# Kernel tuning notes

Hardware: AMD Instinct MI355X
Metric: run time of the kernel (lower is better)

## Reference

```python
import jax, jax.numpy as jnp
import numpy as np
from jax import lax

E = 4        # n_subnets
CAP = 48     # padded per-subnet batch (subnet_bs)
NB = 4       # subnet_num_block (ResBlocks per subnet)
F = 32       # num_feature
RES_SCALE = 0.1


def _conv(x, w, b):
    # x: [B,C,H,W], w: [O,I,3,3] -> SAME conv, NCHW
    y = lax.conv_general_dilated(x, w, (1, 1), 'SAME',
                                 dimension_numbers=('NCHW', 'OIHW', 'NCHW'))
    return y + b[None, :, None, None]


def _pixel_shuffle(x, r):
    B, C, H, W = x.shape
    c = C // (r * r)
    x = x.reshape(B, c, r, r, H, W)
    x = x.transpose(0, 1, 4, 2, 5, 3)          # [B,c,H,r,W,r]
    return x.reshape(B, c, H * r, W * r)


def _subnet(x, hw, hb, r1w, r1b, r2w, r2b, ew, eb, u1w, u1b, u2w, u2b, tw, tb):
    # x: [CAP,3,32,32] -> [CAP,3,128,128]
    h = _conv(x, hw, hb)                        # head
    res = h
    for i in range(NB):                         # ResBlocks: x + s*conv(relu(conv(x)))
        t = jax.nn.relu(_conv(res, r1w[i], r1b[i]))
        res = res + RES_SCALE * _conv(t, r2w[i], r2b[i])
    res = _conv(res, ew, eb) + h                # body_end + skip
    u = _pixel_shuffle(_conv(res, u1w, u1b), 2) # upscale x2
    u = _pixel_shuffle(_conv(u, u2w, u2b), 2)   # upscale x2
    return _conv(u, tw, tb)                     # tail


def setup_inputs() -> dict:
    key = jax.random.key(0)
    ks = jax.random.split(key, 24)

    def w(k, shape, fan_in):
        return jax.random.normal(k, shape, jnp.float32) * (1.0 / np.sqrt(fan_in))

    d = {}
    d['inputs'] = jax.random.normal(ks[0], (128, 3, 32, 32), jnp.float32)
    # classifier: conv3->32 + relu + GAP + linear 32->E
    d['cls_w'] = w(ks[1], (32, 3, 3, 3), 27)
    d['cls_b'] = jnp.zeros((32,), jnp.float32)
    d['cls_fw'] = w(ks[2], (E, 32), 32)
    d['cls_fb'] = jnp.zeros((E,), jnp.float32)
    # stacked per-expert subnet params (leading dim E)
    d['head_w'] = w(ks[3], (E, F, 3, 3, 3), 27)
    d['head_b'] = jnp.zeros((E, F), jnp.float32)
    d['rb_w1'] = w(ks[4], (E, NB, F, F, 3, 3), F * 9)
    d['rb_b1'] = jnp.zeros((E, NB, F), jnp.float32)
    d['rb_w2'] = w(ks[5], (E, NB, F, F, 3, 3), F * 9)
    d['rb_b2'] = jnp.zeros((E, NB, F), jnp.float32)
    d['end_w'] = w(ks[6], (E, F, F, 3, 3), F * 9)
    d['end_b'] = jnp.zeros((E, F), jnp.float32)
    d['up_w1'] = w(ks[7], (E, 4 * F, F, 3, 3), F * 9)
    d['up_b1'] = jnp.zeros((E, 4 * F), jnp.float32)
    d['up_w2'] = w(ks[8], (E, 4 * F, F, 3, 3), F * 9)
    d['up_b2'] = jnp.zeros((E, 4 * F), jnp.float32)
    d['tail_w'] = w(ks[9], (E, 3, F, 3, 3), F * 9)
    d['tail_b'] = jnp.zeros((E, 3), jnp.float32)
    return d


def reference(inputs, cls_w, cls_b, cls_fw, cls_fb, head_w, head_b,
              rb_w1, rb_b1, rb_w2, rb_b2, end_w, end_b,
              up_w1, up_b1, up_w2, up_b2, tail_w, tail_b):
    N = inputs.shape[0]
    # classifier scores -> hard routing (argmax)
    c = jax.nn.relu(_conv(inputs, cls_w, cls_b)).mean((2, 3))   # [N,32]
    scores = c @ cls_fw.T + cls_fb                              # [N,E]
    assign = jnp.argmax(scores, axis=-1)                        # [N]

    # scatter: per-expert sorted position lists, padded to CAP (sentinel N)
    pos = jnp.where(assign[None, :] == jnp.arange(E)[:, None],
                    jnp.arange(N)[None, :], N)                  # [E,N]
    pos = jnp.sort(pos, axis=1)[:, :CAP]                        # [E,CAP]
    valid = pos < N
    safe = jnp.minimum(pos, N - 1)
    x_all = inputs[safe] * valid[:, :, None, None, None]        # [E,CAP,3,32,32]

    # horizontally-fused experts via vmap over expert dim
    y_all = jax.vmap(_subnet)(x_all, head_w, head_b, rb_w1, rb_b1, rb_w2, rb_b2,
                              end_w, end_b, up_w1, up_b1, up_w2, up_b2,
                              tail_w, tail_b)                   # [E,CAP,3,128,128]

    # gather: place real rows back at their original batch positions
    y_all = y_all * valid[:, :, None, None, None]
    out = jnp.zeros((N, 3, 128, 128), y_all.dtype)
    out = out.at[safe.reshape(-1)].add(y_all.reshape(-1, 3, 128, 128))
    return out
```

## Files before the change

kernel.cpp:

```cpp
#include <hip/hip_runtime.h>

#define EXPN 4
#define CAP 48
#define NSLOT 192
#define NBLK 4

#define OFF_RB1 0
#define OFF_RB2 36864
#define OFF_END 73728
#define OFF_UP1 82944
#define OFF_UP2 119808
#define OFF_TAIL 156672
#define PER_E 157536

typedef __attribute__((ext_vector_type(8))) short bf16x8;
typedef __attribute__((ext_vector_type(4))) float f32x4;

static __device__ __forceinline__ float bf2f(unsigned short s) {
  union { unsigned u; float f; } c; c.u = ((unsigned)s) << 16; return c.f;
}
static __device__ __forceinline__ unsigned short f2bf(float f) {
  union { float f; unsigned u; } c; c.f = f;
  unsigned u = c.u;
  return (unsigned short)((u + 0x7fffu + ((u >> 16) & 1u)) >> 16);
}
static __device__ __forceinline__ f32x4 mfma16(bf16x8 a, bf16x8 b, f32x4 c) {
  return __builtin_amdgcn_mfma_f32_16x16x32_bf16(a, b, c, 0, 0, 0);
}
static __device__ __forceinline__ float relu_f(float x) { return fmaxf(x, 0.f); }

static __device__ __forceinline__ unsigned swz(unsigned p, unsigned s) {
  return p * 32 + ((s ^ ((p >> 1) & 3u)) * 8);
}

__global__ void k_zero(float4* __restrict__ p, int n4) {
  int i = blockIdx.x * blockDim.x + threadIdx.x;
  int stride = gridDim.x * blockDim.x;
  for (; i < n4; i += stride) p[i] = make_float4(0.f, 0.f, 0.f, 0.f);
}

__global__ __launch_bounds__(256) void k_wxform(
    const float* __restrict__ rb_w1, const float* __restrict__ rb_w2,
    const float* __restrict__ end_w, const float* __restrict__ up_w1,
    const float* __restrict__ up_w2, const float* __restrict__ tail_w,
    unsigned short* __restrict__ wt) {
  int idx = blockIdx.x * 256 + threadIdx.x;
  if (idx >= EXPN * PER_E) return;
  int e = idx / PER_E, r = idx % PER_E;
  const float* src;
  int c, OC;
  if (r < OFF_RB2) {
    int i = r / 9216; c = r % 9216; OC = 32;
    src = rb_w1 + ((size_t)e * NBLK + i) * 9216;
  } else if (r < OFF_END) {
    int i = (r - OFF_RB2) / 9216; c = (r - OFF_RB2) % 9216; OC = 32;
    src = rb_w2 + ((size_t)e * NBLK + i) * 9216;
  } else if (r < OFF_UP1) {
    c = r - OFF_END; OC = 32;
    src = end_w + (size_t)e * 9216;
  } else if (r < OFF_UP2) {
    c = r - OFF_UP1; OC = 128;
    src = up_w1 + (size_t)e * 36864;
  } else if (r < OFF_TAIL) {
    c = r - OFF_UP2; OC = 128;
    src = up_w2 + (size_t)e * 36864;
  } else {
    c = r - OFF_TAIL; OC = 3;
    src = tail_w + (size_t)e * 864;
  }
  int tap = c / (OC * 32);
  int rem = c % (OC * 32);
  int och = rem / 32, ich = rem % 32;
  wt[idx] = f2bf(src[(och * 32 + ich) * 9 + tap]);
}

__global__ __launch_bounds__(256) void k_cls_conv(
    const float* __restrict__ x, const float* __restrict__ cw,
    const float* __restrict__ cb, float* __restrict__ part) {
  int n = blockIdx.y, band = blockIdx.x, t = threadIdx.x;
  int og = t >> 6, r = (t >> 3) & 7, cg = t & 7;
  int c0 = cg * 4;
  __shared__ float wl[3 * 32 * 9];
  __shared__ float tile[3 * 10 * 34];
  for (int k = t; k < 864; k += 256) {
    int o = k / 27;
    int rem = k % 27;
    int ci = rem / 9, tap = rem % 9;
    wl[(ci * 32 + o) * 9 + tap] = cw[k];
  }
  const float* inb = x + (size_t)n * 3072;
  for (int k = t; k < 1020; k += 256) {
    int ci = k / 340;
    int rem = k % 340;
    int lr = rem / 34, lc = rem % 34;
    int gr = band * 8 - 1 + lr, gc = lc - 1;
    float v = 0.f;
    if (gr >= 0 && gr < 32 && gc >= 0 && gc < 32) v = inb[(ci * 32 + gr) * 32 + gc];
    tile[k] = v;
  }
  __syncthreads();
  float acc[8][4];
#pragma unroll
  for (int oi = 0; oi < 8; ++oi) {
    float b = cb[og * 8 + oi];
#pragma unroll
    for (int p = 0; p < 4; ++p) acc[oi][p] = b;
  }
#pragma unroll
  for (int ci = 0; ci < 3; ++ci) {
    float iv[3][6];
#pragma unroll
    for (int ky = 0; ky < 3; ++ky)
#pragma unroll
      for (int dx = 0; dx < 6; ++dx)
        iv[ky][dx] = tile[ci * 340 + (r + ky) * 34 + c0 + dx];
#pragma unroll
    for (int oi = 0; oi < 8; ++oi) {
      const float* w9 = &wl[((size_t)ci * 32 + og * 8 + oi) * 9];
#pragma unroll
      for (int ky = 0; ky < 3; ++ky)
#pragma unroll
        for (int kx = 0; kx < 3; ++kx) {
          float wv = w9[ky * 3 + kx];
#pragma unroll
          for (int p = 0; p < 4; ++p) acc[oi][p] += wv * iv[ky][p + kx];
        }
    }
  }
#pragma unroll
  for (int oi = 0; oi < 8; ++oi) {
    float s = relu_f(acc[oi][0]) + relu_f(acc[oi][1]) + relu_f(acc[oi][2]) + relu_f(acc[oi][3]);
#pragma unroll
    for (int off = 32; off >= 1; off >>= 1) s += __shfl_down(s, off, 64);
    if ((t & 63) == 0) part[((size_t)n * 4 + band) * 32 + og * 8 + oi] = s;
  }
}

__global__ void k_cls_score(const float* __restrict__ part, const float* __restrict__ fw,
                            const float* __restrict__ fb, int* __restrict__ assign, int N) {
  int n = blockIdx.x * blockDim.x + threadIdx.x;
  if (n >= N) return;
  float cm[32];
#pragma unroll
  for (int o = 0; o < 32; ++o) {
    float s = part[((size_t)n * 4 + 0) * 32 + o] + part[((size_t)n * 4 + 1) * 32 + o] +
              part[((size_t)n * 4 + 2) * 32 + o] + part[((size_t)n * 4 + 3) * 32 + o];
    cm[o] = s * (1.f / 1024.f);
  }
  float best = -1e30f;
  int bi = 0;
  for (int e = 0; e < EXPN; ++e) {
    float sc = fb[e];
#pragma unroll
    for (int o = 0; o < 32; ++o) sc += cm[o] * fw[e * 32 + o];
    if (sc > best) { best = sc; bi = e; }
  }
  assign[n] = bi;
}

__global__ void k_route(const int* __restrict__ assign, int* __restrict__ slot_img, int N) {
  if (threadIdx.x == 0 && blockIdx.x == 0) {
    int cnt[EXPN];
    for (int e = 0; e < EXPN; ++e) cnt[e] = 0;
    for (int k = 0; k < NSLOT; ++k) slot_img[k] = -1;
    for (int n = 0; n < N; ++n) {
      int e = assign[n];
      if (cnt[e] < CAP) { slot_img[e * CAP + cnt[e]] = n; cnt[e]++; }
    }
  }
}

__global__ __launch_bounds__(256) void k_head(
    const float* __restrict__ x, unsigned short* __restrict__ hbuf,
    const float* __restrict__ wglob, const float* __restrict__ bglob,
    const int* __restrict__ slot_img) {
  int slot = blockIdx.y;
  int img = slot_img[slot];
  if (img < 0) return;
  int e = slot / CAP;
  int band = blockIdx.x;
  int t = threadIdx.x;
  int og = t >> 6, r = (t >> 3) & 7, cg = t & 7;
  int c0 = cg * 4;
  __shared__ float wl[3 * 32 * 9];
  __shared__ float tile[3 * 10 * 34];
  __shared__ __align__(16) unsigned short ostg[256 * 32];
  const float* wsrc = wglob + (size_t)e * 32 * 27;
  for (int k = t; k < 864; k += 256) {
    int o = k / 27;
    int rem = k % 27;
    int ci = rem / 9, tap = rem % 9;
    wl[(ci * 32 + o) * 9 + tap] = wsrc[k];
  }
  const float* bsrc = bglob + (size_t)e * 32;
  const float* inb = x + (size_t)img * 3072;
  for (int k = t; k < 3 * 10 * 34; k += 256) {
    int ci = k / 340;
    int rem = k % 340;
    int lr = rem / 34, lc = rem % 34;
    int gr = band * 8 - 1 + lr, gc = lc - 1;
    float v = 0.f;
    if (gr >= 0 && gr < 32 && gc >= 0 && gc < 32) v = inb[(ci * 32 + gr) * 32 + gc];
    tile[k] = v;
  }
  __syncthreads();
  float acc[8][4];
#pragma unroll
  for (int oi = 0; oi < 8; ++oi) {
    float b = bsrc[og * 8 + oi];
#pragma unroll
    for (int p = 0; p < 4; ++p) acc[oi][p] = b;
  }
#pragma unroll
  for (int ci = 0; ci < 3; ++ci) {
    float iv[3][6];
#pragma unroll
    for (int ky = 0; ky < 3; ++ky)
#pragma unroll
      for (int dx = 0; dx < 6; ++dx)
        iv[ky][dx] = tile[ci * 340 + (r + ky) * 34 + c0 + dx];
#pragma unroll
    for (int oi = 0; oi < 8; ++oi) {
      const float* w9 = &wl[((size_t)ci * 32 + og * 8 + oi) * 9];
#pragma unroll
      for (int ky = 0; ky < 3; ++ky)
#pragma unroll
        for (int kx = 0; kx < 3; ++kx) {
          float wv = w9[ky * 3 + kx];
#pragma unroll
          for (int p = 0; p < 4; ++p) acc[oi][p] += wv * iv[ky][p + kx];
        }
    }
  }
#pragma unroll
  for (int oi = 0; oi < 8; ++oi)
#pragma unroll
    for (int p = 0; p < 4; ++p)
      ostg[(r * 32 + c0 + p) * 32 + og * 8 + oi] = f2bf(acc[oi][p]);
  __syncthreads();
  for (int u = t; u < 1024; u += 256) {
    int px = u >> 2, c8 = (u & 3) * 8;
    int4 v = *(const int4*)&ostg[px * 32 + c8];
    size_t gi = ((size_t)slot * 1024 + band * 256 + px) * 32 + c8;
    *(int4*)&hbuf[gi] = v;
  }
}

template <int EPI>
static __device__ __forceinline__ void conv32_lds8(
    const unsigned short* __restrict__ srcP, unsigned short* __restrict__ dstP,
    const unsigned short* __restrict__ hb,
    const unsigned short* __restrict__ wtc, const float* __restrict__ bsrc,
    const int (&rdA)[6][3], const int (&wrA)[4][2],
    int w, int l, int col, int s4) {
  bf16x8 Bf[9][2];
  f32x4 bias4[2];
#pragma unroll
  for (int n = 0; n < 2; ++n) {
    bias4[n] = *(const f32x4*)&bsrc[n * 16 + s4 * 4];
#pragma unroll
    for (int tap = 0; tap < 9; ++tap)
      Bf[tap][n] = *(const bf16x8*)&wtc[((tap * 32) + n * 16 + col) * 32 + s4 * 8];
  }
  int rbase = w * 4;
#pragma unroll
  for (int xh = 0; xh < 2; ++xh) {
    bf16x8 Af[6][3];
#pragma unroll
    for (int rr = 0; rr < 6; ++rr)
#pragma unroll
      for (int kx = 0; kx < 3; ++kx)
        Af[rr][kx] = *(const bf16x8*)&srcP[rdA[rr][kx] + xh * 512];
    f32x4 acc[4][2];
#pragma unroll
    for (int m = 0; m < 4; ++m)
#pragma unroll
      for (int n = 0; n < 2; ++n) acc[m][n] = bias4[n];
    __builtin_amdgcn_s_setprio(1);
#pragma unroll
    for (int ky = 0; ky < 3; ++ky)
#pragma unroll
      for (int kx = 0; kx < 3; ++kx)
#pragma unroll
        for (int r = 0; r < 4; ++r)
#pragma unroll
          for (int n = 0; n < 2; ++n)
            acc[r][n] = mfma16(Bf[ky * 3 + kx][n], Af[r + ky][kx], acc[r][n]);
    __builtin_amdgcn_s_setprio(0);
#pragma unroll
    for (int r = 0; r < 4; ++r) {
      int row = rbase + r;
      int x = xh * 16 + col;
#pragma unroll
      for (int n = 0; n < 2; ++n) {
        unsigned li = (unsigned)(wrA[r][n] + xh * 512);
        float v0 = acc[r][n][0], v1 = acc[r][n][1], v2 = acc[r][n][2], v3 = acc[r][n][3];
        if (EPI == 0) {
          v0 = relu_f(v0); v1 = relu_f(v1); v2 = relu_f(v2); v3 = relu_f(v3);
        } else if (EPI == 1) {
          uint2 old = *(const uint2*)&dstP[li];
          v0 = bf2f((unsigned short)(old.x & 0xffff)) + 0.1f * v0;
          v1 = bf2f((unsigned short)(old.x >> 16)) + 0.1f * v1;
          v2 = bf2f((unsigned short)(old.y & 0xffff)) + 0.1f * v2;
          v3 = bf2f((unsigned short)(old.y >> 16)) + 0.1f * v3;
        } else if (EPI == 2) {
          uint2 hv = *(const uint2*)&hb[((unsigned)(row * 32 + x)) * 32 + n * 16 + s4 * 4];
          v0 += bf2f((unsigned short)(hv.x & 0xffff));
          v1 += bf2f((unsigned short)(hv.x >> 16));
          v2 += bf2f((unsigned short)(hv.y & 0xffff));
          v3 += bf2f((unsigned short)(hv.y >> 16));
        }
        uint2 o;
        o.x = (unsigned)f2bf(v0) | ((unsigned)f2bf(v1) << 16);
        o.y = (unsigned)f2bf(v2) | ((unsigned)f2bf(v3) << 16);
        *(uint2*)&dstP[li] = o;
      }
    }
  }
}

__global__ __launch_bounds__(512, 1) void k_body(
    const unsigned short* __restrict__ hbuf, unsigned short* __restrict__ u1,
    const unsigned short* __restrict__ wt,
    const float* __restrict__ rb_b1, const float* __restrict__ rb_b2,
    const float* __restrict__ end_b, const float* __restrict__ up_b1,
    const int* __restrict__ slot_img) {
  int slot = blockIdx.x;
  int img = slot_img[slot];
  if (img < 0) return;
  int e = slot / CAP;
  int t = threadIdx.x;
  int w = t >> 6, l = t & 63;
  int col = l & 15, s4 = l >> 4;

  __shared__ __align__(16) unsigned short resP[34 * 34 * 32];
  __shared__ __align__(16) unsigned short tP[34 * 34 * 32];
  __shared__ __align__(16) unsigned short scr[8 * 512];

  int rdA[6][3];
  int wrA[4][2];
#pragma unroll
  for (int rr = 0; rr < 6; ++rr)
#pragma unroll
    for (int kx = 0; kx < 3; ++kx)
      rdA[rr][kx] = (int)swz((unsigned)((w * 4 + rr) * 34 + col + kx), (unsigned)s4);
#pragma unroll
  for (int r = 0; r < 4; ++r)
#pragma unroll
    for (int n = 0; n < 2; ++n)
      wrA[r][n] = (int)(swz((unsigned)((w * 4 + r + 1) * 34 + col + 1),
                            (unsigned)(n * 2 + (s4 >> 1))) + (s4 & 1) * 4);

  int4 z = make_int4(0, 0, 0, 0);
  for (int u = t; u < 4624; u += 512) {
    *(int4*)&resP[u * 8] = z;
    *(int4*)&tP[u * 8] = z;
  }
  __syncthreads();
  const unsigned short* hsl = hbuf + (size_t)slot * 32768;
  for (int u = t; u < 4096; u += 512) {
    int px = u >> 2, sl = u & 3;
    unsigned p = (unsigned)(((px >> 5) + 1) * 34 + (px & 31) + 1);
    *(int4*)&resP[swz(p, sl)] = *(const int4*)&hsl[px * 32 + sl * 8];
  }
  __syncthreads();

  unsigned short* wscr = &scr[w * 512];
  const unsigned short* wte = wt + (size_t)e * PER_E;

  for (int i = 0; i < NBLK; ++i) {
    conv32_lds8<0>(resP, tP, nullptr, wte + OFF_RB1 + i * 9216,
                   rb_b1 + (size_t)e * NBLK * 32 + i * 32, rdA, wrA, w, l, col, s4);
    __syncthreads();
    conv32_lds8<1>(tP, resP, nullptr, wte + OFF_RB2 + i * 9216,
                   rb_b2 + (size_t)e * NBLK * 32 + i * 32, rdA, wrA, w, l, col, s4);
    __syncthreads();
  }
  conv32_lds8<2>(resP, tP, hsl, wte + OFF_END, end_b + (size_t)e * 32, rdA, wrA,
                 w, l, col, s4);
  __syncthreads();

  {
    int og = w >> 1, rh = w & 1;
    const unsigned short* wtc = wte + OFF_UP1;
    const float* bsrc = up_b1 + (size_t)e * 128;
    bf16x8 Bf[9][2];
    float bias[2];
#pragma unroll
    for (int n = 0; n < 2; ++n) {
      int och = og * 32 + n * 16 + col;
      bias[n] = bsrc[och];
#pragma unroll
      for (int tap = 0; tap < 9; ++tap)
        Bf[tap][n] = *(const bf16x8*)&wtc[((tap * 128) + och) * 32 + s4 * 8];
    }
    unsigned short* u1g = u1 + (size_t)slot * 64 * 64 * 32;
#pragma unroll
    for (int xh = 0; xh < 2; ++xh) {
      int x0 = xh * 16;
#pragma unroll
      for (int rg = 0; rg < 4; ++rg) {
        int rbase = rh * 16 + rg * 4;
        bf16x8 Af[6][3];
#pragma unroll
        for (int rr = 0; rr < 6; ++rr)
#pragma unroll
          for (int kx = 0; kx < 3; ++kx)
            Af[rr][kx] = *(const bf16x8*)&tP[swz((rbase + rr) * 34 + x0 + col + kx, s4)];
        f32x4 acc[4][2];
#pragma unroll
        for (int m = 0; m < 4; ++m)
#pragma unroll
          for (int n = 0; n < 2; ++n) acc[m][n] = (f32x4){bias[n], bias[n], bias[n], bias[n]};
        __builtin_amdgcn_s_setprio(1);
#pragma unroll
        for (int ky = 0; ky < 3; ++ky)
#pragma unroll
          for (int kx = 0; kx < 3; ++kx)
#pragma unroll
            for (int r = 0; r < 4; ++r)
#pragma unroll
              for (int n = 0; n < 2; ++n)
                acc[r][n] = mfma16(Af[r + ky][kx], Bf[ky * 3 + kx][n], acc[r][n]);
        __builtin_amdgcn_s_setprio(0);
#pragma unroll
        for (int r = 0; r < 4; ++r) {
          int row = rbase + r;
#pragma unroll
          for (int n = 0; n < 2; ++n) {
            int och = og * 32 + n * 16 + col;
            int ryrx = och & 3, ccl = (och >> 2) & 7;
#pragma unroll
            for (int reg = 0; reg < 4; ++reg)
              wscr[(ryrx * 16 + s4 * 4 + reg) * 8 + ccl] = f2bf(acc[r][n][reg]);
          }
          int ryrx2 = l >> 4, px2 = l & 15;
          int4 yv = *(const int4*)&wscr[(ryrx2 * 16 + px2) * 8];
          int ry = ryrx2 >> 1, rx = ryrx2 & 1;
          int oy = 2 * row + ry, ox = 2 * (x0 + px2) + rx;
          *(int4*)&u1g[((size_t)oy * 64 + ox) * 32 + og * 8] = yv;
        }
      }
    }
  }
}

__global__ __launch_bounds__(256) void k_uptail(
    const unsigned short* __restrict__ u1, float* __restrict__ out,
    const unsigned short* __restrict__ wt, const float* __restrict__ up_b2,
    const float* __restrict__ tail_b, const int* __restrict__ slot_img) {
  int slot = blockIdx.y;
  int img = slot_img[slot];
  if (img < 0) return;
  int e = slot / CAP;
  int b = blockIdx.x & 15;
  int xh2 = blockIdx.x >> 4;
  int t = threadIdx.x;
  int w = t >> 6, l = t & 63;
  int col = l & 15, s4 = l >> 4;

  __shared__ __align__(16) unsigned short u1t[8 * 36 * 32];
  __shared__ __align__(16) unsigned short u2t[10 * 66 * 32];

  const unsigned short* u1s = u1 + (size_t)slot * 64 * 64 * 32;
  int r0 = 4 * b - 2, c0g = 32 * xh2 - 2;
  for (int u = t; u < 8 * 36 * 4; u += 256) {
    int rr = u / 144;
    int rem = u - rr * 144;
    int cc = rem >> 2, sl = rem & 3;
    int gy = r0 + rr, gx = c0g + cc;
    int4 v = make_int4(0, 0, 0, 0);
    if (gy >= 0 && gy < 64 && gx >= 0 && gx < 64)
      v = *(const int4*)&u1s[((size_t)gy * 64 + gx) * 32 + sl * 8];
    *(int4*)&u1t[swz((unsigned)(rr * 36 + cc), sl)] = v;
  }

  const unsigned short* wtc = wt + (size_t)e * PER_E + OFF_UP2;
  bf16x8 Bf[9][2];
  f32x4 bias4[2];
#pragma unroll
  for (int n = 0; n < 2; ++n) {
    bias4[n] = *(const f32x4*)&up_b2[(size_t)e * 128 + w * 32 + n * 16 + s4 * 4];
#pragma unroll
    for (int tap = 0; tap < 9; ++tap)
      Bf[tap][n] = *(const bf16x8*)&wtc[((tap * 128) + w * 32 + n * 16 + col) * 32 + s4 * 8];
  }
  const unsigned short* wtt = wt + (size_t)e * PER_E + OFF_TAIL;
  bf16x8 Bt[9];
  float biast = 0.f;
  if (col < 3) biast = tail_b[e * 3 + col];
#pragma unroll
  for (int tap = 0; tap < 9; ++tap) {
    if (col < 3)
      Bt[tap] = *(const bf16x8*)&wtt[((tap * 3) + col) * 32 + s4 * 8];
    else {
      bf16x8 bb;
#pragma unroll
      for (int j = 0; j < 8; ++j) bb[j] = (short)0;
      Bt[tap] = bb;
    }
  }
  __syncthreads();

#pragma unroll
  for (int xg = 0; xg < 3; ++xg) {
    int xl = xg * 16 + col;
    bf16x8 Af[3][3];
#pragma unroll
    for (int rr = 0; rr < 3; ++rr)
#pragma unroll
      for (int kx = 0; kx < 3; ++kx)
        Af[rr][kx] = *(const bf16x8*)&u1t[swz((unsigned)(rr * 36 + xg * 16 + col + kx), s4)];
#pragma unroll
    for (int yy = 0; yy < 6; ++yy) {
      if (yy > 0) {
#pragma unroll
        for (int kx = 0; kx < 3; ++kx)
          Af[(yy + 2) % 3][kx] =
              *(const bf16x8*)&u1t[swz((unsigned)((yy + 2) * 36 + xg * 16 + col + kx), s4)];
      }
      f32x4 acc[2];
#pragma unroll
      for (int n = 0; n < 2; ++n) acc[n] = bias4[n];
      __builtin_amdgcn_s_setprio(1);
#pragma unroll
      for (int ky = 0; ky < 3; ++ky)
#pragma unroll
        for (int kx = 0; kx < 3; ++kx)
#pragma unroll
          for (int n = 0; n < 2; ++n)
            acc[n] = mfma16(Bf[ky * 3 + kx][n], Af[(yy + ky) % 3][kx], acc[n]);
      __builtin_amdgcn_s_setprio(0);
#pragma unroll
      for (int n = 0; n < 2; ++n)
#pragma unroll
        for (int reg = 0; reg < 4; ++reg) {
          int ry = reg >> 1, rx = reg & 1;
          int oyl = 2 * yy + ry - 1;
          int oxl = 2 * xl + rx - 1;
          if (oyl >= 0 && oyl < 10 && oxl >= 0 && oxl < 66) {
            int gy2 = 8 * b - 1 + oyl;
            int gx2 = 64 * xh2 - 1 + oxl;
            float v = (gy2 >= 0 && gy2 < 128 && gx2 >= 0 && gx2 < 128) ? acc[n][reg] : 0.f;
            u2t[swz((unsigned)(oyl * 66 + oxl), (unsigned)w) + n * 4 + s4] = f2bf(v);
          }
        }
    }
  }
  __syncthreads();

#pragma unroll
  for (int gx = 0; gx < 4; ++gx) {
    bf16x8 At[4][3];
#pragma unroll
    for (int rr = 0; rr < 4; ++rr)
#pragma unroll
      for (int kx = 0; kx < 3; ++kx)
        At[rr][kx] = *(const bf16x8*)&u2t[swz((w * 2 + rr) * 66 + gx * 16 + col + kx, s4)];
    f32x4 acc[2];
#pragma unroll
    for (int r = 0; r < 2; ++r) acc[r] = (f32x4){biast, biast, biast, biast};
    __builtin_amdgcn_s_setprio(1);
#pragma unroll
    for (int ky = 0; ky < 3; ++ky)
#pragma unroll
      for (int kx = 0; kx < 3; ++kx)
#pragma unroll
        for (int r = 0; r < 2; ++r)
          acc[r] = mfma16(At[r + ky][kx], Bt[ky * 3 + kx], acc[r]);
    __builtin_amdgcn_s_setprio(0);
    if (col < 3) {
#pragma unroll
      for (int r = 0; r < 2; ++r) {
        int grow = 8 * b + w * 2 + r;
        int gcol = 64 * xh2 + gx * 16 + s4 * 4;
        *(float4*)&out[(((size_t)img * 3 + col) * 128 + grow) * 128 + gcol] =
            make_float4(acc[r][0], acc[r][1], acc[r][2], acc[r][3]);
      }
    }
  }
}

extern "C" void kernel_launch(void* const* d_in, const int* in_sizes, int n_in,
                              void* d_out, int out_size, void* d_ws, size_t ws_size,
                              hipStream_t stream) {
  const float* inputs = (const float*)d_in[0];
  const float* cls_w = (const float*)d_in[1];
  const float* cls_b = (const float*)d_in[2];
  const float* cls_fw = (const float*)d_in[3];
  const float* cls_fb = (const float*)d_in[4];
  const float* head_w = (const float*)d_in[5];
  const float* head_b = (const float*)d_in[6];
  const float* rb_w1 = (const float*)d_in[7];
  const float* rb_b1 = (const float*)d_in[8];
  const float* rb_w2 = (const float*)d_in[9];
  const float* rb_b2 = (const float*)d_in[10];
  const float* end_w = (const float*)d_in[11];
  const float* end_b = (const float*)d_in[12];
  const float* up_w1 = (const float*)d_in[13];
  const float* up_b1 = (const float*)d_in[14];
  const float* up_w2 = (const float*)d_in[15];
  const float* up_b2 = (const float*)d_in[16];
  const float* tail_w = (const float*)d_in[17];
  const float* tail_b = (const float*)d_in[18];
  float* out = (float*)d_out;
  char* ws = (char*)d_ws;

  int N = in_sizes[0] / 3072;

  int* assign = (int*)ws;
  int* slot_img = (int*)(ws + 512);
  float* part = (float*)(ws + 4096);
  unsigned short* wt = (unsigned short*)(ws + 131072);
  const size_t ABUF = (size_t)NSLOT * 1024 * 32 * 2;
  size_t o_h = 1572864;
  unsigned short* h = (unsigned short*)(ws + o_h);
  unsigned short* u1 = (unsigned short*)(ws + o_h + ABUF);

  k_zero<<<2048, 256, 0, stream>>>((float4*)out, out_size / 4);
  k_wxform<<<(EXPN * PER_E + 255) / 256, 256, 0, stream>>>(
      rb_w1, rb_w2, end_w, up_w1, up_w2, tail_w, wt);
  k_cls_conv<<<dim3(4, N), 256, 0, stream>>>(inputs, cls_w, cls_b, part);
  k_cls_score<<<(N + 63) / 64, 64, 0, stream>>>(part, cls_fw, cls_fb, assign, N);
  k_route<<<1, 64, 0, stream>>>(assign, slot_img, N);

  k_head<<<dim3(4, NSLOT), 256, 0, stream>>>(inputs, h, head_w, head_b, slot_img);

  k_body<<<NSLOT, 512, 0, stream>>>(h, u1, wt, rb_b1, rb_b2, end_b, up_b1, slot_img);

  k_uptail<<<dim3(32, NSLOT), 256, 0, stream>>>(u1, out, wt, up_b2, tail_b, slot_img);
}
```

Before: 184.8 us.

## Fuse launch-overhead kernels and precompute LDS addresses in uptail

Folds the weight transform into k_head, merges scoring and routing into one single-block kernel, and replaces the full output zero-fill with zeroing only rows of unrouted images. In k_uptail, swizzled LDS addresses are precomputed into registers and the bounds checks on the u2 store are simplified into compile-time-resolvable conditions. This cuts the number of launches and the output memset traffic, at the cost of more registers in k_uptail and a serial single-block zeroing path when images overflow capacity.

```diff
diff --git a/kernel.cpp b/kernel.cpp
--- a/kernel.cpp
+++ b/kernel.cpp
@@ -32,46 +32,8 @@
 static __device__ __forceinline__ unsigned swz(unsigned p, unsigned s) {
   return p * 32 + ((s ^ ((p >> 1) & 3u)) * 8);
 }
-
-__global__ void k_zero(float4* __restrict__ p, int n4) {
-  int i = blockIdx.x * blockDim.x + threadIdx.x;
-  int stride = gridDim.x * blockDim.x;
-  for (; i < n4; i += stride) p[i] = make_float4(0.f, 0.f, 0.f, 0.f);
-}
-
-__global__ __launch_bounds__(256) void k_wxform(
-    const float* __restrict__ rb_w1, const float* __restrict__ rb_w2,
-    const float* __restrict__ end_w, const float* __restrict__ up_w1,
-    const float* __restrict__ up_w2, const float* __restrict__ tail_w,
-    unsigned short* __restrict__ wt) {
-  int idx = blockIdx.x * 256 + threadIdx.x;
-  if (idx >= EXPN * PER_E) return;
-  int e = idx / PER_E, r = idx % PER_E;
-  const float* src;
-  int c, OC;
-  if (r < OFF_RB2) {
-    int i = r / 9216; c = r % 9216; OC = 32;
-    src = rb_w1 + ((size_t)e * NBLK + i) * 9216;
-  } else if (r < OFF_END) {
-    int i = (r - OFF_RB2) / 9216; c = (r - OFF_RB2) % 9216; OC = 32;
-    src = rb_w2 + ((size_t)e * NBLK + i) * 9216;
-  } else if (r < OFF_UP1) {
-    c = r - OFF_END; OC = 32;
-    src = end_w + (size_t)e * 9216;
-  } else if (r < OFF_UP2) {
-    c = r - OFF_UP1; OC = 128;
-    src = up_w1 + (size_t)e * 36864;
-  } else if (r < OFF_TAIL) {
-    c = r - OFF_UP2; OC = 128;
-    src = up_w2 + (size_t)e * 36864;
-  } else {
-    c = r - OFF_TAIL; OC = 3;
-    src = tail_w + (size_t)e * 864;
-  }
-  int tap = c / (OC * 32);
-  int rem = c % (OC * 32);
-  int och = rem / 32, ich = rem % 32;
-  wt[idx] = f2bf(src[(och * 32 + ich) * 9 + tap]);
+static __device__ __forceinline__ int swzI(int p, int s) {
+  return p * 32 + ((s ^ ((p >> 1) & 3)) * 8);
 }
 
 __global__ __launch_bounds__(256) void k_cls_conv(
@@ -136,36 +98,47 @@
   }
 }
 
-__global__ void k_cls_score(const float* __restrict__ part, const float* __restrict__ fw,
-                            const float* __restrict__ fb, int* __restrict__ assign, int N) {
-  int n = blockIdx.x * blockDim.x + threadIdx.x;
-  if (n >= N) return;
-  float cm[32];
-#pragma unroll
-  for (int o = 0; o < 32; ++o) {
-    float s = part[((size_t)n * 4 + 0) * 32 + o] + part[((size_t)n * 4 + 1) * 32 + o] +
-              part[((size_t)n * 4 + 2) * 32 + o] + part[((size_t)n * 4 + 3) * 32 + o];
-    cm[o] = s * (1.f / 1024.f);
-  }
-  float best = -1e30f;
-  int bi = 0;
-  for (int e = 0; e < EXPN; ++e) {
-    float sc = fb[e];
-#pragma unroll
-    for (int o = 0; o < 32; ++o) sc += cm[o] * fw[e * 32 + o];
-    if (sc > best) { best = sc; bi = e; }
-  }
-  assign[n] = bi;
-}
-
-__global__ void k_route(const int* __restrict__ assign, int* __restrict__ slot_img, int N) {
-  if (threadIdx.x == 0 && blockIdx.x == 0) {
+__global__ __launch_bounds__(256) void k_score_route(
+    const float* __restrict__ part, const float* __restrict__ fw,
+    const float* __restrict__ fb, int* __restrict__ slot_img,
+    float* __restrict__ out, int N) {
+  __shared__ int assign_s[256];
+  __shared__ unsigned char routed_s[256];
+  int t = threadIdx.x;
+  routed_s[t] = 0;
+  for (int n = t; n < N; n += 256) {
+    float cm[32];
+#pragma unroll
+    for (int o = 0; o < 32; ++o) {
+      float s = part[((size_t)n * 4 + 0) * 32 + o] + part[((size_t)n * 4 + 1) * 32 + o] +
+                part[((size_t)n * 4 + 2) * 32 + o] + part[((size_t)n * 4 + 3) * 32 + o];
+      cm[o] = s * (1.f / 1024.f);
+    }
+    float best = -1e30f;
+    int bi = 0;
+    for (int e = 0; e < EXPN; ++e) {
+      float sc = fb[e];
+#pragma unroll
+      for (int o = 0; o < 32; ++o) sc += cm[o] * fw[e * 32 + o];
+      if (sc > best) { best = sc; bi = e; }
+    }
+    assign_s[n] = bi;
+  }
+  __syncthreads();
+  if (t == 0) {
     int cnt[EXPN];
     for (int e = 0; e < EXPN; ++e) cnt[e] = 0;
     for (int k = 0; k < NSLOT; ++k) slot_img[k] = -1;
     for (int n = 0; n < N; ++n) {
-      int e = assign[n];
-      if (cnt[e] < CAP) { slot_img[e * CAP + cnt[e]] = n; cnt[e]++; }
+      int e = assign_s[n];
+      if (cnt[e] < CAP) { slot_img[e * CAP + cnt[e]] = n; cnt[e]++; routed_s[n] = 1; }
+    }
+  }
+  __syncthreads();
+  for (int n = 0; n < N; ++n) {
+    if (!routed_s[n]) {
+      float4* o = (float4*)(out + (size_t)n * 49152);
+      for (int i = t; i < 12288; i += 256) o[i] = make_float4(0.f, 0.f, 0.f, 0.f);
     }
   }
 }
@@ -173,13 +146,48 @@
 __global__ __launch_bounds__(256) void k_head(
     const float* __restrict__ x, unsigned short* __restrict__ hbuf,
     const float* __restrict__ wglob, const float* __restrict__ bglob,
-    const int* __restrict__ slot_img) {
+    const int* __restrict__ slot_img,
+    const float* __restrict__ rb_w1, const float* __restrict__ rb_w2,
+    const float* __restrict__ end_w, const float* __restrict__ up_w1,
+    const float* __restrict__ up_w2, const float* __restrict__ tail_w,
+    unsigned short* __restrict__ wt) {
   int slot = blockIdx.y;
+  int band = blockIdx.x;
+  int t = threadIdx.x;
+  {
+    int bid = blockIdx.y * 4 + blockIdx.x;
+    for (int idx = bid * 256 + t; idx < EXPN * PER_E; idx += 768 * 256) {
+      int e = idx / PER_E, r = idx % PER_E;
+      const float* src;
+      int c, OC;
+      if (r < OFF_RB2) {
+        int i = r / 9216; c = r % 9216; OC = 32;
+        src = rb_w1 + ((size_t)e * NBLK + i) * 9216;
+      } else if (r < OFF_END) {
+        int i = (r - OFF_RB2) / 9216; c = (r - OFF_RB2) % 9216; OC = 32;
+        src = rb_w2 + ((size_t)e * NBLK + i) * 9216;
+      } else if (r < OFF_UP1) {
+        c = r - OFF_END; OC = 32;
+        src = end_w + (size_t)e * 9216;
+      } else if (r < OFF_UP2) {
+        c = r - OFF_UP1; OC = 128;
+        src = up_w1 + (size_t)e * 36864;
+      } else if (r < OFF_TAIL) {
+        c = r - OFF_UP2; OC = 128;
+        src = up_w2 + (size_t)e * 36864;
+      } else {
+        c = r - OFF_TAIL; OC = 3;
+        src = tail_w + (size_t)e * 864;
+      }
+      int tap = c / (OC * 32);
+      int rem = c % (OC * 32);
+      int och = rem / 32, ich = rem % 32;
+      wt[idx] = f2bf(src[(och * 32 + ich) * 9 + tap]);
+    }
+  }
   int img = slot_img[slot];
   if (img < 0) return;
   int e = slot / CAP;
-  int band = blockIdx.x;
-  int t = threadIdx.x;
   int og = t >> 6, r = (t >> 3) & 7, cg = t & 7;
   int c0 = cg * 4;
   __shared__ float wl[3 * 32 * 9];
@@ -462,6 +470,30 @@
   __shared__ __align__(16) unsigned short u1t[8 * 36 * 32];
   __shared__ __align__(16) unsigned short u2t[10 * 66 * 32];
 
+  int rdU[2][3];
+#pragma unroll
+  for (int rp = 0; rp < 2; ++rp)
+#pragma unroll
+    for (int kx = 0; kx < 3; ++kx)
+      rdU[rp][kx] = (int)swz((unsigned)(rp * 36 + col + kx), (unsigned)s4);
+  int stB[2][2][4];
+#pragma unroll
+  for (int yp = 0; yp < 2; ++yp)
+#pragma unroll
+    for (int n = 0; n < 2; ++n)
+#pragma unroll
+      for (int reg = 0; reg < 4; ++reg) {
+        int ry = reg >> 1, rx = reg & 1;
+        int pb = (2 * yp + ry - 1) * 66 + 2 * col + rx - 1;
+        stB[yp][n][reg] = swzI(pb, w) + n * 4 + s4;
+      }
+  int rdT[4][3];
+#pragma unroll
+  for (int rr = 0; rr < 4; ++rr)
+#pragma unroll
+    for (int kx = 0; kx < 3; ++kx)
+      rdT[rr][kx] = (int)swz((unsigned)((w * 2 + rr) * 66 + col + kx), (unsigned)s4);
+
   const unsigned short* u1s = u1 + (size_t)slot * 64 * 64 * 32;
   int r0 = 4 * b - 2, c0g = 32 * xh2 - 2;
   for (int u = t; u < 8 * 36 * 4; u += 256) {
@@ -504,20 +536,20 @@
 
 #pragma unroll
   for (int xg = 0; xg < 3; ++xg) {
-    int xl = xg * 16 + col;
     bf16x8 Af[3][3];
 #pragma unroll
     for (int rr = 0; rr < 3; ++rr)
 #pragma unroll
       for (int kx = 0; kx < 3; ++kx)
-        Af[rr][kx] = *(const bf16x8*)&u1t[swz((unsigned)(rr * 36 + xg * 16 + col + kx), s4)];
+        Af[rr][kx] = *(const bf16x8*)&u1t[rdU[rr & 1][kx] + (rr >> 1) * 2304 + xg * 512];
 #pragma unroll
     for (int yy = 0; yy < 6; ++yy) {
       if (yy > 0) {
+        int row = yy + 2;
 #pragma unroll
         for (int kx = 0; kx < 3; ++kx)
           Af[(yy + 2) % 3][kx] =
-              *(const bf16x8*)&u1t[swz((unsigned)((yy + 2) * 36 + xg * 16 + col + kx), s4)];
+              *(const bf16x8*)&u1t[rdU[row & 1][kx] + (row >> 1) * 2304 + xg * 512];
       }
       f32x4 acc[2];
 #pragma unroll
@@ -536,14 +568,16 @@
 #pragma unroll
         for (int reg = 0; reg < 4; ++reg) {
           int ry = reg >> 1, rx = reg & 1;
-          int oyl = 2 * yy + ry - 1;
-          int oxl = 2 * xl + rx - 1;
-          if (oyl >= 0 && oyl < 10 && oxl >= 0 && oxl < 66) {
-            int gy2 = 8 * b - 1 + oyl;
-            int gx2 = 64 * xh2 - 1 + oxl;
-            float v = (gy2 >= 0 && gy2 < 128 && gx2 >= 0 && gx2 < 128) ? acc[n][reg] : 0.f;
-            u2t[swz((unsigned)(oyl * 66 + oxl), (unsigned)w) + n * 4 + s4] = f2bf(v);
-          }
+          if ((yy == 0 && ry == 0) || (yy == 5 && ry == 1)) continue;
+          bool valid = (xg == 1) || (xg == 0 && (col > 0 || rx == 1)) ||
+                       (xg == 2 && (2 * col + rx <= 2));
+          float v = acc[n][reg];
+          if (b == 0 && yy == 0 && ry == 1) v = 0.f;
+          if (b == 15 && yy == 5 && ry == 0) v = 0.f;
+          if (xh2 == 0 && xg == 0 && col == 0 && rx == 1) v = 0.f;
+          if (xh2 == 1 && xg == 2 && col == 1 && rx == 0) v = 0.f;
+          if (valid)
+            u2t[(unsigned)(stB[yy & 1][n][reg] + (yy >> 1) * 8448 + xg * 1024)] = f2bf(v);
         }
     }
   }
@@ -556,7 +590,7 @@
     for (int rr = 0; rr < 4; ++rr)
 #pragma unroll
       for (int kx = 0; kx < 3; ++kx)
-        At[rr][kx] = *(const bf16x8*)&u2t[swz((w * 2 + rr) * 66 + gx * 16 + col + kx, s4)];
+        At[rr][kx] = *(const bf16x8*)&u2t[rdT[rr][kx] + gx * 512];
     f32x4 acc[2];
 #pragma unroll
     for (int r = 0; r < 2; ++r) acc[r] = (f32x4){biast, biast, biast, biast};
@@ -608,7 +642,6 @@
 
   int N = in_sizes[0] / 3072;
 
-  int* assign = (int*)ws;
   int* slot_img = (int*)(ws + 512);
   float* part = (float*)(ws + 4096);
   unsigned short* wt = (unsigned short*)(ws + 131072);
@@ -617,14 +650,11 @@
   unsigned short* h = (unsigned short*)(ws + o_h);
   unsigned short* u1 = (unsigned short*)(ws + o_h + ABUF);
 
-  k_zero<<<2048, 256, 0, stream>>>((float4*)out, out_size / 4);
-  k_wxform<<<(EXPN * PER_E + 255) / 256, 256, 0, stream>>>(
-      rb_w1, rb_w2, end_w, up_w1, up_w2, tail_w, wt);
   k_cls_conv<<<dim3(4, N), 256, 0, stream>>>(inputs, cls_w, cls_b, part);
-  k_cls_score<<<(N + 63) / 64, 64, 0, stream>>>(part, cls_fw, cls_fb, assign, N);
-  k_route<<<1, 64, 0, stream>>>(assign, slot_img, N);
-
-  k_head<<<dim3(4, NSLOT), 256, 0, stream>>>(inputs, h, head_w, head_b, slot_img);
+  k_score_route<<<1, 256, 0, stream>>>(part, cls_fw, cls_fb, slot_img, out, N);
+
+  k_head<<<dim3(4, NSLOT), 256, 0, stream>>>(inputs, h, head_w, head_b, slot_img,
+                                             rb_w1, rb_w2, end_w, up_w1, up_w2, tail_w, wt);
 
   k_body<<<NSLOT, 512, 0, stream>>>(h, u1, wt, rb_b1, rb_b2, end_b, up_b1, slot_img);
 
```

After: 263.7 us. +42.7%, slower.
